# Kernel optimization log

Hardware: AMD Instinct MI355X
Metric: run time of the kernel (lower is better)

Reference implementation:

```python
import jax, jax.numpy as jnp
import numpy as np

A, B, O, C = 8, 32768, 256, 64   # num_agents, batch, obs_size, action_size
E, H = 128, 4                     # embedding_dim, attention_heads
Dh = E // H                       # attend_dim = 32
EPS = 1e-5                        # BatchNorm1d eps
SLOPE = 0.01                      # LeakyReLU default negative slope


def lrelu(x):
    return jnp.where(x >= 0, x, SLOPE * x)


def batchnorm(x, gamma, beta):
    # x: [A,B,F]; training-mode BatchNorm1d per agent (biased batch variance)
    mu = x.mean(axis=1, keepdims=True)
    var = x.var(axis=1, keepdims=True)
    return (x - mu) / jnp.sqrt(var + EPS) * gamma[:, None, :] + beta[:, None, :]


def setup_inputs() -> dict:
    key = jax.random.key(0)
    ks = jax.random.split(key, 13)
    s = lambda k, shape: jax.random.normal(k, shape, jnp.float32) * 0.05
    return {
        "observation_vector": jax.random.normal(ks[0], (A, B, O), jnp.float32),
        "action_vector": jax.random.normal(ks[1], (A, B, C), jnp.float32),
        "g_bn_gamma": jnp.ones((A, O + C), jnp.float32),
        "g_bn_beta": jnp.zeros((A, O + C), jnp.float32),
        "g_W": s(ks[2], (A, E, O + C)), "g_b": s(ks[3], (A, E)),
        "s_bn_gamma": jnp.ones((A, O), jnp.float32),
        "s_bn_beta": jnp.zeros((A, O), jnp.float32),
        "s_W": s(ks[4], (A, E, O)), "s_b": s(ks[5], (A, E)),
        "f_W1": s(ks[6], (A, E, 2 * E)), "f_b1": s(ks[7], (A, E)),
        "f_W2": s(ks[8], (A, C, E)), "f_b2": s(ks[9], (A, C)),
        "Wq": s(ks[10], (H, Dh, E)), "Wk": s(ks[11], (H, Dh, E)),
        "V": s(ks[12], (H, Dh, E)),
    }


def reference(observation_vector, action_vector, g_bn_gamma, g_bn_beta, g_W, g_b,
              s_bn_gamma, s_bn_beta, s_W, s_b, f_W1, f_b1, f_W2, f_b2, Wq, Wk, V):
    # per-agent embeddings of (obs, act) and obs-only
    combined = jnp.concatenate([observation_vector, action_vector], axis=2)      # [A,B,O+C]
    e = lrelu(jnp.einsum('abf,aef->abe', batchnorm(combined, g_bn_gamma, g_bn_beta), g_W)
              + g_b[:, None, :])                                                  # [A,B,E]
    si = lrelu(jnp.einsum('abf,aef->abe',
                          batchnorm(observation_vector, s_bn_gamma, s_bn_beta), s_W)
               + s_b[:, None, :])                                                 # [A,B,E]
    # NOTE: original applies F.softmax over a (batch,1) tensor -> every attention
    # weight is exactly 1.0, so x_i = sum_{j!=i} leaky_relu(V_l @ e_j). Wq/Wk only
    # feed the regularization logits (not returned when regularize=False).
    v = lrelu(jnp.einsum('abe,hde->abhd', e, V))                                  # [A,B,H,Dh]
    x = (v.sum(axis=0, keepdims=True) - v).reshape(A, B, E)                       # heads concatenated
    h = lrelu(jnp.einsum('abf,aef->abe', jnp.concatenate([x, si], axis=2), f_W1)
              + f_b1[:, None, :])                                                 # [A,B,E]
    q_all = jnp.einsum('abe,ace->abc', h, f_W2) + f_b2[:, None, :]                # [A,B,C]
    ids = jnp.argmax(action_vector, axis=2)[..., None]                            # [A,B,1]
    return jnp.take_along_axis(q_all, ids, axis=2)                                # [A,B,1]
```

## Files before the change

### kernel.cpp

```cpp
#include <hip/hip_runtime.h>
#include <hip/hip_bf16.h>
#include <stdint.h>

constexpr int A_ = 8, B_ = 32768, O_ = 256, C_ = 64, F_ = 320, E_ = 128;
constexpr int NCH = 128, CHROWS = B_ / NCH;
constexpr int NBT = B_ / 16;

typedef __attribute__((ext_vector_type(8))) __bf16 bf16x8;
typedef __attribute__((ext_vector_type(4))) float f32x4;
union U4 { uint4 u; bf16x8 v; __bf16 b[8]; };

__device__ __forceinline__ float lrelu(float x){ return x >= 0.f ? x : 0.01f*x; }
__device__ __forceinline__ f32x4 mfma16(bf16x8 a, bf16x8 b, f32x4 c){
  return __builtin_amdgcn_mfma_f32_16x16x32_bf16(a, b, c, 0, 0, 0);
}
__device__ __forceinline__ bf16x8 pk8(f32x4 lo, f32x4 hi){
  U4 r;
  r.b[0]=(__bf16)lo[0]; r.b[1]=(__bf16)lo[1]; r.b[2]=(__bf16)lo[2]; r.b[3]=(__bf16)lo[3];
  r.b[4]=(__bf16)hi[0]; r.b[5]=(__bf16)hi[1]; r.b[6]=(__bf16)hi[2]; r.b[7]=(__bf16)hi[3];
  return r.v;
}
__device__ __forceinline__ bf16x8 pk8f(float4 a, float4 b){
  U4 r;
  r.b[0]=(__bf16)a.x; r.b[1]=(__bf16)a.y; r.b[2]=(__bf16)a.z; r.b[3]=(__bf16)a.w;
  r.b[4]=(__bf16)b.x; r.b[5]=(__bf16)b.y; r.b[6]=(__bf16)b.z; r.b[7]=(__bf16)b.w;
  return r.v;
}
__device__ __forceinline__ void gl_lds16(const void* g, void* s){
  __builtin_amdgcn_global_load_lds(
      (const __attribute__((address_space(1))) unsigned int*)g,
      (__attribute__((address_space(3))) unsigned int*)s, 16, 0, 0);
}
template<int N> __device__ __forceinline__ void vmwait(){
  asm volatile("s_waitcnt vmcnt(%0)" :: "n"(N) : "memory");
}
__device__ __forceinline__ void lgkm0(){ asm volatile("s_waitcnt lgkmcnt(0)" ::: "memory"); }
__device__ __forceinline__ void sbar(){ __builtin_amdgcn_s_barrier(); }
__device__ __forceinline__ void schb(){ __builtin_amdgcn_sched_barrier(0); }

__global__ void k_stats_partial(const float* __restrict__ obs,
                                const float* __restrict__ act,
                                float* __restrict__ psum, float* __restrict__ psq,
                                int* __restrict__ ids){
  const int f = threadIdx.x, ch = blockIdx.x, a = blockIdx.y;
  const size_t b0 = (size_t)ch * CHROWS;
  float s = 0.f, q = 0.f;
  if (f < O_){
    const float* p = obs + ((size_t)a*B_ + b0)*O_ + f;
    for (int i = 0; i < CHROWS; ++i){ float x = p[(size_t)i*O_]; s += x; q += x*x; }
  } else {
    const float* p = act + ((size_t)a*B_ + b0)*C_ + (f - O_);
    for (int i = 0; i < CHROWS; ++i){ float x = p[(size_t)i*C_]; s += x; q += x*x; }
  }
  psum[((size_t)a*NCH + ch)*F_ + f] = s;
  psq [((size_t)a*NCH + ch)*F_ + f] = q;
  if (f < CHROWS){
    const float4* ar = (const float4*)(act + ((size_t)a*B_ + b0 + f)*C_);
    float best = -3.4e38f; int bi = 0;
    #pragma unroll 4
    for (int j = 0; j < 16; ++j){
      const float4 v = ar[j];
      const int c0 = j*4;
      if (v.x > best){ best = v.x; bi = c0;   }
      if (v.y > best){ best = v.y; bi = c0+1; }
      if (v.z > best){ best = v.z; bi = c0+2; }
      if (v.w > best){ best = v.w; bi = c0+3; }
    }
    ids[(size_t)a*B_ + b0 + f] = bi;
  }
}

__global__ void k_stats_final(const float* __restrict__ psum, const float* __restrict__ psq,
                              float* __restrict__ zscale, float* __restrict__ zshift){
  const int f = threadIdx.x, a = blockIdx.x;
  float s = 0.f, q = 0.f;
  for (int ch = 0; ch < NCH; ++ch){
    s += psum[((size_t)a*NCH + ch)*F_ + f];
    q += psq [((size_t)a*NCH + ch)*F_ + f];
  }
  const float mean = s * (1.0f / B_);
  float var = q * (1.0f / B_) - mean * mean;
  var = fmaxf(var, 0.0f);
  const float rs = rsqrtf(var + 1e-5f);
  zscale[a*F_ + f] = rs;
  zshift[a*F_ + f] = -mean * rs;
}

__global__ void k_prep_pack(const float* __restrict__ gW, const float* __restrict__ ggam,
                            const float* __restrict__ sW, const float* __restrict__ sgam,
                            const float* __restrict__ f1W, const float* __restrict__ f2W,
                            const float* __restrict__ Vm, const float* __restrict__ zscale,
                            __bf16* __restrict__ Ap, __bf16* __restrict__ Vp,
                            __bf16* __restrict__ B1p, __bf16* __restrict__ B2p){
  const int a = blockIdx.y;
  const int t0 = blockIdx.x*256 + threadIdx.x;
  constexpr int STR = 32*256;
  for (int i = t0; i < 10*16*64*8; i += STR){
    const int ks = i >> 13, mO = (i>>9)&15, l = (i>>3)&63, e = i&7;
    const int lg = l>>4, fo = mO*16 + (l&15), k = ks*32 + lg*8 + e;
    const float sc = zscale[a*F_ + k];
    float v;
    if (fo < 128) v = gW[(size_t)a*E_*F_ + (size_t)fo*F_ + k] * ggam[a*F_+k] * sc;
    else          v = (k < O_) ? sW[(size_t)a*E_*O_ + (size_t)(fo-128)*O_ + k] * sgam[a*O_+k] * sc : 0.f;
    Ap[(size_t)a*(10*16*64*8) + i] = (__bf16)v;
  }
  for (int i = t0; i < 8*8*64*8; i += STR){
    const int ks = i >> 12, mH = (i>>9)&7, l = (i>>3)&63, e = i&7;
    const int lg = l>>4, h = mH*16 + (l&15);
    const int f = 32*ks + 16*(e>>2) + 4*lg + (e&3);
    B1p[(size_t)a*(8*8*64*8) + i] = (__bf16)f1W[(size_t)a*E_*2*E_ + (size_t)h*2*E_ + f];
  }
  for (int i = t0; i < 4*4*64*8; i += STR){
    const int ks = i >> 11, mC = (i>>9)&3, l = (i>>3)&63, e = i&7;
    const int lg = l>>4, c = mC*16 + (l&15);
    const int f = 32*ks + 16*(e>>2) + 4*lg + (e&3);
    B2p[(size_t)a*(4*4*64*8) + i] = (__bf16)f2W[(size_t)a*C_*E_ + (size_t)c*E_ + f];
  }
  if (a == 0){
    for (int i = t0; i < 4*8*64*8; i += STR){
      const int ks = i >> 12, mV = (i>>9)&7, l = (i>>3)&63, e = i&7;
      const int lg = l>>4, vo = mV*16 + (l&15);
      const int f = 32*ks + 16*(e>>2) + 4*lg + (e&3);
      Vp[i] = (__bf16)Vm[(size_t)vo*E_ + f];
    }
  }
}

__global__ void k_prep_bias(const float* __restrict__ gW, const float* __restrict__ gb,
                            const float* __restrict__ ggam, const float* __restrict__ gbet,
                            const float* __restrict__ sW, const float* __restrict__ sb,
                            const float* __restrict__ sgam, const float* __restrict__ sbet,
                            const float* __restrict__ zshift, float* __restrict__ gsb){
  __shared__ float ww[F_];
  __shared__ float part[2][128];
  const int a = blockIdx.y, t = threadIdx.x;
  const int o = t & 127, h = t >> 7;
  if (blockIdx.x == 0){
    for (int f = t; f < F_; f += 256)
      ww[f] = gbet[a*F_+f] + ggam[a*F_+f]*zshift[a*F_+f];
    __syncthreads();
    float s = 0.f;
    #pragma unroll 4
    for (int f = h*160; f < h*160 + 160; f += 4){
      const float4 wv = *(const float4*)&gW[(size_t)a*E_*F_ + (size_t)o*F_ + f];
      s += wv.x*ww[f] + wv.y*ww[f+1] + wv.z*ww[f+2] + wv.w*ww[f+3];
    }
    part[h][o] = s;
    __syncthreads();
    if (t < 128) gsb[a*256 + t] = gb[a*E_+t] + part[0][t] + part[1][t];
  } else {
    for (int f = t; f < O_; f += 256)
      ww[f] = sbet[a*O_+f] + sgam[a*O_+f]*zshift[a*F_+f];
    __syncthreads();
    float s = 0.f;
    #pragma unroll 4
    for (int f = h*128; f < h*128 + 128; f += 4){
      const float4 wv = *(const float4*)&sW[(size_t)a*E_*O_ + (size_t)o*O_ + f];
      s += wv.x*ww[f] + wv.y*ww[f+1] + wv.z*ww[f+2] + wv.w*ww[f+3];
    }
    part[h][o] = s;
    __syncthreads();
    if (t < 128) gsb[a*256 + 128 + t] = sb[a*E_+t] + part[0][t] + part[1][t];
  }
}

__global__ __launch_bounds__(256, 2) void k_stageA(
    const float* __restrict__ obs, const float* __restrict__ act,
    const __bf16* __restrict__ Ap, const __bf16* __restrict__ Vp,
    const float* __restrict__ gsb,
    uint4* __restrict__ si_q, uint4* __restrict__ v_q){
  constexpr int BUF = 26624;
  __shared__ __align__(16) char smem[2*BUF];
  const int a = (A_-1) - blockIdx.y;
  const int t = threadIdx.x;
  const int w = t>>6, l = t&63, l15 = l&15, lg = l>>4;
  const int bt0 = ((NBT/8 - 1) - blockIdx.x)*8;
  const size_t grow0 = (size_t)a*B_ + (size_t)bt0*16;
  const char* ApA = (const char*)Ap + (size_t)a*163840;
  const int xr = t>>1, kc0 = (t&1)*2;
  const float* obsrow = obs + (grow0 + xr)*O_;
  const float* actrow = act + (grow0 + xr)*C_;

  float4 xA[4], xB[4];

  auto wstage = [&](int ks, char* buf){
    const char* src = ApA + ks*16384;
    #pragma unroll
    for (int i = 0; i < 4; ++i)
      gl_lds16(src + (w*4+i)*1024 + l*16, buf + (w*4+i)*1024);
  };
  auto xload = [&](int ks, float4* d){
    const float* s = (ks < 8) ? (obsrow + ks*32 + kc0*8) : (actrow + (ks-8)*32 + kc0*8);
    d[0] = ((const float4*)s)[0]; d[1] = ((const float4*)s)[1];
    d[2] = ((const float4*)s)[2]; d[3] = ((const float4*)s)[3];
  };
  auto xwrite = [&](char* buf, const float4* d){
    *(bf16x8*)(buf + 16384 + xr*80 + kc0*16)     = pk8f(d[0], d[1]);
    *(bf16x8*)(buf + 16384 + xr*80 + (kc0+1)*16) = pk8f(d[2], d[3]);
  };

  f32x4 acc[4][8] = {};

  wstage(0, smem); schb();
  xload(0, xA);
  vmwait<0>();
  xwrite(smem, xA);
  xload(1, xB);
  lgkm0(); sbar(); schb();

  #pragma unroll
  for (int ks = 0; ks < 10; ++ks){
    char* cur = smem + (ks&1)*BUF;
    char* nxt = smem + ((ks+1)&1)*BUF;
    if (ks+1 < 10){ wstage(ks+1, nxt); schb(); }
    if (ks+2 < 10) xload(ks+2, (ks&1) ? xB : xA);
    {
      const bf16x8* wc = (const bf16x8*)cur;
      const char* xb = cur + 16384;
      bf16x8 bfr[8];
      #pragma unroll
      for (int nt = 0; nt < 8; ++nt)
        bfr[nt] = *(const bf16x8*)(xb + (nt*16 + l15)*80 + lg*16);
      #pragma unroll
      for (int m = 0; m < 4; ++m){
        const bf16x8 af = wc[(w*4+m)*64 + l];
        #pragma unroll
        for (int nt = 0; nt < 8; ++nt)
          acc[m][nt] = mfma16(af, bfr[nt], acc[m][nt]);
      }
    }
    schb();
    if (ks <= 7)      vmwait<4>();
    else if (ks == 8) vmwait<0>();
    if (ks+1 < 10) xwrite(nxt, (ks&1) ? xA : xB);
    if (ks < 9){ lgkm0(); sbar(); schb(); }
  }

  const float* bE = gsb + a*256 + w*64 + lg*4;
  #pragma unroll
  for (int m = 0; m < 4; ++m){
    const float4 b = *(const float4*)(bE + m*16);
    #pragma unroll
    for (int nt = 0; nt < 8; ++nt){
      acc[m][nt][0] = lrelu(acc[m][nt][0] + b.x);
      acc[m][nt][1] = lrelu(acc[m][nt][1] + b.y);
      acc[m][nt][2] = lrelu(acc[m][nt][2] + b.z);
      acc[m][nt][3] = lrelu(acc[m][nt][3] + b.w);
    }
  }
  sbar();

  if (w < 2){
    #pragma unroll
    for (int jp = 0; jp < 2; ++jp){
      const int kv = 2*w + jp;
      #pragma unroll
      for (int nt = 0; nt < 8; ++nt)
        *(bf16x8*)(smem + ((kv*8 + nt)*64 + l)*16) = pk8(acc[2*jp][nt], acc[2*jp+1][nt]);
    }
  } else {
    #pragma unroll
    for (int jp = 0; jp < 2; ++jp){
      const int j = 2*(w-2) + jp;
      #pragma unroll
      for (int nt = 0; nt < 8; ++nt){
        U4 u; u.v = pk8(acc[2*jp][nt], acc[2*jp+1][nt]);
        si_q[(((size_t)a*NBT + bt0 + nt)*4 + j)*64 + l] = u.u;
      }
    }
  }
  lgkm0(); sbar(); schb();

  const uint4* Vq = (const uint4*)Vp;
  f32x4 accv[2][8] = {};
  #pragma unroll
  for (int kv = 0; kv < 4; ++kv){
    U4 a0, a1;
    a0.u = Vq[(kv*8 + w*2 + 0)*64 + l];
    a1.u = Vq[(kv*8 + w*2 + 1)*64 + l];
    bf16x8 bv[8];
    #pragma unroll
    for (int nt = 0; nt < 8; ++nt)
      bv[nt] = *(const bf16x8*)(smem + ((kv*8 + nt)*64 + l)*16);
    #pragma unroll
    for (int nt = 0; nt < 8; ++nt){
      accv[0][nt] = mfma16(a0.v, bv[nt], accv[0][nt]);
      accv[1][nt] = mfma16(a1.v, bv[nt], accv[1][nt]);
    }
  }
  #pragma unroll
  for (int nt = 0; nt < 8; ++nt){
    f32x4 lo, hi;
    #pragma unroll
    for (int e = 0; e < 4; ++e){ lo[e] = lrelu(accv[0][nt][e]); hi[e] = lrelu(accv[1][nt][e]); }
    U4 u; u.v = pk8(lo, hi);
    v_q[(((size_t)a*NBT + bt0 + nt)*4 + w)*64 + l] = u.u;
  }
}

__global__ void k_vsum(const uint4* __restrict__ v_q, uint4* __restrict__ vsum_q){
  const size_t i = (size_t)blockIdx.x*256 + threadIdx.x;
  const size_t per_a = (size_t)NBT*4*64;
  float s[8] = {0,0,0,0,0,0,0,0};
  #pragma unroll
  for (int aa = 0; aa < 8; ++aa){
    U4 u; u.u = v_q[aa*per_a + i];
    #pragma unroll
    for (int e = 0; e < 8; ++e) s[e] += (float)u.b[e];
  }
  U4 o;
  #pragma unroll
  for (int e = 0; e < 8; ++e) o.b[e] = (__bf16)s[e];
  vsum_q[i] = o.u;
}

__global__ __launch_bounds__(256, 2) void k_stageC(
    const uint4* __restrict__ v_q, const uint4* __restrict__ si_q,
    const uint4* __restrict__ vsum_q,
    const __bf16* __restrict__ B1p, const __bf16* __restrict__ B2p,
    const float* __restrict__ f1b, const float* __restrict__ f2b,
    const int* __restrict__ ids, float* __restrict__ out){
  __shared__ __align__(16) char wsm[2*8192];
  __shared__ float qs[4][64][17];
  const int a = blockIdx.y, t = threadIdx.x;
  const int w = t>>6, l = t&63, l15 = l&15, lg = l>>4;
  const int btw = blockIdx.x*8 + w*2;
  const char* B1A = (const char*)B1p + (size_t)a*65536;
  const size_t vbase = (size_t)a*NBT*4*64;

  uint4 qA[2], qB[2], sA[2], sB[2];

  auto wstage = [&](int ks, char* dst){
    const char* src = B1A + ks*8192;
    #pragma unroll
    for (int i = 0; i < 2; ++i)
      gl_lds16(src + (w*2+i)*1024 + l*16, dst + (w*2+i)*1024);
  };
  auto bload = [&](int ks, uint4* qv, uint4* sv){
    if (ks < 4){
      #pragma unroll
      for (int nt = 0; nt < 2; ++nt){
        const size_t idx = ((size_t)(btw+nt)*4 + ks)*64 + l;
        qv[nt] = v_q[vbase + idx];
        sv[nt] = vsum_q[idx];
      }
    } else {
      #pragma unroll
      for (int nt = 0; nt < 2; ++nt)
        qv[nt] = si_q[vbase + ((size_t)(btw+nt)*4 + (ks-4))*64 + l];
    }
  };
  auto bmake = [&](int ks, const uint4* qv, const uint4* sv, bf16x8* bf){
    if (ks < 4){
      #pragma unroll
      for (int nt = 0; nt < 2; ++nt){
        U4 s, v; s.u = sv[nt]; v.u = qv[nt];
        f32x4 lo, hi;
        #pragma unroll
        for (int e = 0; e < 4; ++e){
          lo[e] = (float)s.b[e]   - (float)v.b[e];
          hi[e] = (float)s.b[e+4] - (float)v.b[e+4];
        }
        bf[nt] = pk8(lo, hi);
      }
    } else {
      #pragma unroll
      for (int nt = 0; nt < 2; ++nt){ U4 u; u.u = qv[nt]; bf[nt] = u.v; }
    }
  };

  f32x4 hacc[8][2] = {};
  wstage(0, wsm); schb();
  bload(0, qA, sA); schb();
  bload(1, qB, sB);
  vmwait<4>();
  sbar(); schb();

  #pragma unroll
  for (int ks = 0; ks < 8; ++ks){
    bf16x8 bf[2];
    bmake(ks, (ks&1) ? qB : qA, (ks&1) ? sB : sA, bf);
    if (ks+1 < 8){ wstage(ks+1, wsm + ((ks+1)&1)*8192); schb(); }
    if (ks+2 < 8) bload(ks+2, (ks&1) ? qB : qA, (ks&1) ? sB : sA);
    {
      const bf16x8* wc = (const bf16x8*)(wsm + (ks&1)*8192);
      #pragma unroll
      for (int m = 0; m < 8; ++m){
        const bf16x8 af = wc[m*64 + l];
        hacc[m][0] = mfma16(af, bf[0], hacc[m][0]);
        hacc[m][1] = mfma16(af, bf[1], hacc[m][1]);
      }
    }
    schb();
    if (ks <= 1)      vmwait<4>();
    else if (ks <= 5) vmwait<2>();
    else if (ks == 6) vmwait<0>();
    if (ks < 7){ sbar(); schb(); }
  }

  bf16x8 hb[4][2];
  const float* bH = f1b + a*E_ + lg*4;
  #pragma unroll
  for (int kq = 0; kq < 4; ++kq){
    const float4 b0v = *(const float4*)(bH + (2*kq)*16);
    const float4 b1v = *(const float4*)(bH + (2*kq+1)*16);
    #pragma unroll
    for (int nt = 0; nt < 2; ++nt){
      f32x4 lo, hi;
      lo[0]=lrelu(hacc[2*kq][nt][0]+b0v.x); lo[1]=lrelu(hacc[2*kq][nt][1]+b0v.y);
      lo[2]=lrelu(hacc[2*kq][nt][2]+b0v.z); lo[3]=lrelu(hacc[2*kq][nt][3]+b0v.w);
      hi[0]=lrelu(hacc[2*kq+1][nt][0]+b1v.x); hi[1]=lrelu(hacc[2*kq+1][nt][1]+b1v.y);
      hi[2]=lrelu(hacc[2*kq+1][nt][2]+b1v.z); hi[3]=lrelu(hacc[2*kq+1][nt][3]+b1v.w);
      hb[kq][nt] = pk8(lo, hi);
    }
  }
  const uint4* A2q = (const uint4*)(B2p + (size_t)a*(4*4*64*8));
  f32x4 accq[4][2] = {};
  #pragma unroll
  for (int kq = 0; kq < 4; ++kq){
    #pragma unroll
    for (int mC = 0; mC < 4; ++mC){
      U4 af; af.u = A2q[(kq*4 + mC)*64 + l];
      accq[mC][0] = mfma16(af.v, hb[kq][0], accq[mC][0]);
      accq[mC][1] = mfma16(af.v, hb[kq][1], accq[mC][1]);
    }
  }
  const float* bQ = f2b + a*C_ + lg*4;
  float4 qb[4];
  #pragma unroll
  for (int mC = 0; mC < 4; ++mC) qb[mC] = *(const float4*)(bQ + mC*16);
  #pragma unroll
  for (int nt = 0; nt < 2; ++nt){
    #pragma unroll
    for (int mC = 0; mC < 4; ++mC){
      qs[w][mC*16 + lg*4 + 0][l15] = accq[mC][nt][0] + qb[mC].x;
      qs[w][mC*16 + lg*4 + 1][l15] = accq[mC][nt][1] + qb[mC].y;
      qs[w][mC*16 + lg*4 + 2][l15] = accq[mC][nt][2] + qb[mC].z;
      qs[w][mC*16 + lg*4 + 3][l15] = accq[mC][nt][3] + qb[mC].w;
    }
    lgkm0();
    if (l < 16){
      const size_t row = (size_t)(btw + nt)*16 + l;
      const int id = ids[(size_t)a*B_ + row];
      out[(size_t)a*B_ + row] = qs[w][id][l];
    }
    lgkm0();
  }
}

extern "C" void kernel_launch(void* const* d_in, const int* in_sizes, int n_in,
                              void* d_out, int out_size, void* d_ws, size_t ws_size,
                              hipStream_t stream) {
  const float* obs  = (const float*)d_in[0];
  const float* act  = (const float*)d_in[1];
  const float* ggam = (const float*)d_in[2];
  const float* gbet = (const float*)d_in[3];
  const float* gW   = (const float*)d_in[4];
  const float* gb   = (const float*)d_in[5];
  const float* sgam = (const float*)d_in[6];
  const float* sbet = (const float*)d_in[7];
  const float* sW   = (const float*)d_in[8];
  const float* sb   = (const float*)d_in[9];
  const float* f1W  = (const float*)d_in[10];
  const float* f1b  = (const float*)d_in[11];
  const float* f2W  = (const float*)d_in[12];
  const float* f2b  = (const float*)d_in[13];
  const float* Vm   = (const float*)d_in[16];
  float* out = (float*)d_out;

  char* base = (char*)d_ws; size_t off = 0;
  auto alloc = [&](size_t bytes) -> void* {
    off = (off + 255) & ~(size_t)255; void* p = base + off; off += bytes; return p;
  };
  float* psum    = (float*)alloc((size_t)A_*NCH*F_*4);
  float* psq     = (float*)alloc((size_t)A_*NCH*F_*4);
  float* zscale  = (float*)alloc((size_t)A_*F_*4);
  float* zshift  = (float*)alloc((size_t)A_*F_*4);
  float* gsb     = (float*)alloc((size_t)A_*256*4);
  __bf16* Ap     = (__bf16*)alloc((size_t)A_*10*16*64*8*2);
  __bf16* Vp     = (__bf16*)alloc((size_t)4*8*64*8*2);
  __bf16* B1p    = (__bf16*)alloc((size_t)A_*8*8*64*8*2);
  __bf16* B2p    = (__bf16*)alloc((size_t)A_*4*4*64*8*2);
  uint4* si_q    = (uint4*)alloc((size_t)A_*NBT*4*64*16);
  uint4* v_q     = (uint4*)alloc((size_t)A_*NBT*4*64*16);
  uint4* vsum_q  = (uint4*)alloc((size_t)NBT*4*64*16);
  int*   ids     = (int*)alloc((size_t)A_*B_*4);
  (void)ws_size; (void)in_sizes; (void)n_in; (void)out_size;

  k_stats_partial<<<dim3(NCH, A_), 320, 0, stream>>>(obs, act, psum, psq, ids);
  k_stats_final<<<A_, F_, 0, stream>>>(psum, psq, zscale, zshift);
  k_prep_pack<<<dim3(32, A_), 256, 0, stream>>>(gW, ggam, sW, sgam, f1W, f2W, Vm,
                                                zscale, Ap, Vp, B1p, B2p);
  k_prep_bias<<<dim3(2, A_), 256, 0, stream>>>(gW, gb, ggam, gbet, sW, sb, sgam, sbet,
                                               zshift, gsb);
  k_stageA<<<dim3(NBT/8, A_), 256, 0, stream>>>(obs, act, Ap, Vp, gsb, si_q, v_q);
  k_vsum<<<(NBT*4*64)/256, 256, 0, stream>>>(v_q, vsum_q);
  k_stageC<<<dim3(NBT/8, A_), 256, 0, stream>>>(v_q, si_q, vsum_q, B1p, B2p,
                                                f1b, f2b, ids, out);
}
```

Before: 257.1 us.

## Replace hand-tuned software pipelining with simple syncthreads-based loops

Stage A drops the two-deep register prefetch of activations, the explicit vmcnt waits and the sched barriers, and uses one register buffer plus __syncthreads each step. Stage C drops LDS staging of the f_W1 weights and the register double buffering, and reads weights and activations straight from global memory inside the k loop. This makes the code simpler and lowers LDS use, but it gives up explicit overlap of memory latency with MFMA work. It also adds full block barriers in the output gather.

```diff
diff --git a/kernel.cpp b/kernel.cpp
--- a/kernel.cpp
+++ b/kernel.cpp
@@ -31,12 +31,6 @@
       (const __attribute__((address_space(1))) unsigned int*)g,
       (__attribute__((address_space(3))) unsigned int*)s, 16, 0, 0);
 }
-template<int N> __device__ __forceinline__ void vmwait(){
-  asm volatile("s_waitcnt vmcnt(%0)" :: "n"(N) : "memory");
-}
-__device__ __forceinline__ void lgkm0(){ asm volatile("s_waitcnt lgkmcnt(0)" ::: "memory"); }
-__device__ __forceinline__ void sbar(){ __builtin_amdgcn_s_barrier(); }
-__device__ __forceinline__ void schb(){ __builtin_amdgcn_sched_barrier(0); }
 
 __global__ void k_stats_partial(const float* __restrict__ obs,
                                 const float* __restrict__ act,
@@ -181,7 +175,7 @@
   const float* obsrow = obs + (grow0 + xr)*O_;
   const float* actrow = act + (grow0 + xr)*C_;
 
-  float4 xA[4], xB[4];
+  float4 xr4[4];
 
   auto wstage = [&](int ks, char* buf){
     const char* src = ApA + ks*16384;
@@ -201,19 +195,19 @@
 
   f32x4 acc[4][8] = {};
 
-  wstage(0, smem); schb();
-  xload(0, xA);
-  vmwait<0>();
-  xwrite(smem, xA);
-  xload(1, xB);
-  lgkm0(); sbar(); schb();
+  wstage(0, smem);
+  xload(0, xr4);
+  xwrite(smem, xr4);
+  __syncthreads();
 
   #pragma unroll
   for (int ks = 0; ks < 10; ++ks){
     char* cur = smem + (ks&1)*BUF;
     char* nxt = smem + ((ks+1)&1)*BUF;
-    if (ks+1 < 10){ wstage(ks+1, nxt); schb(); }
-    if (ks+2 < 10) xload(ks+2, (ks&1) ? xB : xA);
+    if (ks+1 < 10){
+      wstage(ks+1, nxt);
+      xload(ks+1, xr4);
+    }
     {
       const bf16x8* wc = (const bf16x8*)cur;
       const char* xb = cur + 16384;
@@ -229,11 +223,8 @@
           acc[m][nt] = mfma16(af, bfr[nt], acc[m][nt]);
       }
     }
-    schb();
-    if (ks <= 7)      vmwait<4>();
-    else if (ks == 8) vmwait<0>();
-    if (ks+1 < 10) xwrite(nxt, (ks&1) ? xA : xB);
-    if (ks < 9){ lgkm0(); sbar(); schb(); }
+    if (ks+1 < 10) xwrite(nxt, xr4);
+    __syncthreads();
   }
 
   const float* bE = gsb + a*256 + w*64 + lg*4;
@@ -248,8 +239,6 @@
       acc[m][nt][3] = lrelu(acc[m][nt][3] + b.w);
     }
   }
-  sbar();
-
   if (w < 2){
     #pragma unroll
     for (int jp = 0; jp < 2; ++jp){
@@ -269,7 +258,7 @@
       }
     }
   }
-  lgkm0(); sbar(); schb();
+  __syncthreads();
 
   const uint4* Vq = (const uint4*)Vp;
   f32x4 accv[2][8] = {};
@@ -320,41 +309,22 @@
     const __bf16* __restrict__ B1p, const __bf16* __restrict__ B2p,
     const float* __restrict__ f1b, const float* __restrict__ f2b,
     const int* __restrict__ ids, float* __restrict__ out){
-  __shared__ __align__(16) char wsm[2*8192];
   __shared__ float qs[4][64][17];
   const int a = blockIdx.y, t = threadIdx.x;
   const int w = t>>6, l = t&63, l15 = l&15, lg = l>>4;
   const int btw = blockIdx.x*8 + w*2;
-  const char* B1A = (const char*)B1p + (size_t)a*65536;
+  const uint4* B1q = (const uint4*)(B1p + (size_t)a*(8*8*64*8));
   const size_t vbase = (size_t)a*NBT*4*64;
 
-  uint4 qA[2], qB[2], sA[2], sB[2];
-
-  auto wstage = [&](int ks, char* dst){
-    const char* src = B1A + ks*8192;
-    #pragma unroll
-    for (int i = 0; i < 2; ++i)
-      gl_lds16(src + (w*2+i)*1024 + l*16, dst + (w*2+i)*1024);
-  };
-  auto bload = [&](int ks, uint4* qv, uint4* sv){
+  f32x4 hacc[8][2] = {};
+  #pragma unroll
+  for (int ks = 0; ks < 8; ++ks){
+    bf16x8 bf[2];
     if (ks < 4){
       #pragma unroll
       for (int nt = 0; nt < 2; ++nt){
         const size_t idx = ((size_t)(btw+nt)*4 + ks)*64 + l;
-        qv[nt] = v_q[vbase + idx];
-        sv[nt] = vsum_q[idx];
-      }
-    } else {
-      #pragma unroll
-      for (int nt = 0; nt < 2; ++nt)
-        qv[nt] = si_q[vbase + ((size_t)(btw+nt)*4 + (ks-4))*64 + l];
-    }
-  };
-  auto bmake = [&](int ks, const uint4* qv, const uint4* sv, bf16x8* bf){
-    if (ks < 4){
-      #pragma unroll
-      for (int nt = 0; nt < 2; ++nt){
-        U4 s, v; s.u = sv[nt]; v.u = qv[nt];
+        U4 s, v; v.u = v_q[vbase + idx]; s.u = vsum_q[idx];
         f32x4 lo, hi;
         #pragma unroll
         for (int e = 0; e < 4; ++e){
@@ -365,37 +335,17 @@
       }
     } else {
       #pragma unroll
-      for (int nt = 0; nt < 2; ++nt){ U4 u; u.u = qv[nt]; bf[nt] = u.v; }
-    }
-  };
-
-  f32x4 hacc[8][2] = {};
-  wstage(0, wsm); schb();
-  bload(0, qA, sA); schb();
-  bload(1, qB, sB);
-  vmwait<4>();
-  sbar(); schb();
-
-  #pragma unroll
-  for (int ks = 0; ks < 8; ++ks){
-    bf16x8 bf[2];
-    bmake(ks, (ks&1) ? qB : qA, (ks&1) ? sB : sA, bf);
-    if (ks+1 < 8){ wstage(ks+1, wsm + ((ks+1)&1)*8192); schb(); }
-    if (ks+2 < 8) bload(ks+2, (ks&1) ? qB : qA, (ks&1) ? sB : sA);
-    {
-      const bf16x8* wc = (const bf16x8*)(wsm + (ks&1)*8192);
-      #pragma unroll
-      for (int m = 0; m < 8; ++m){
-        const bf16x8 af = wc[m*64 + l];
-        hacc[m][0] = mfma16(af, bf[0], hacc[m][0]);
-        hacc[m][1] = mfma16(af, bf[1], hacc[m][1]);
+      for (int nt = 0; nt < 2; ++nt){
+        U4 u; u.u = si_q[vbase + ((size_t)(btw+nt)*4 + (ks-4))*64 + l];
+        bf[nt] = u.v;
       }
     }
-    schb();
-    if (ks <= 1)      vmwait<4>();
-    else if (ks <= 5) vmwait<2>();
-    else if (ks == 6) vmwait<0>();
-    if (ks < 7){ sbar(); schb(); }
+    #pragma unroll
+    for (int m = 0; m < 8; ++m){
+      U4 af; af.u = B1q[(ks*8 + m)*64 + l];
+      hacc[m][0] = mfma16(af.v, bf[0], hacc[m][0]);
+      hacc[m][1] = mfma16(af.v, bf[1], hacc[m][1]);
+    }
   }
 
   bf16x8 hb[4][2];
@@ -438,13 +388,13 @@
       qs[w][mC*16 + lg*4 + 2][l15] = accq[mC][nt][2] + qb[mC].z;
       qs[w][mC*16 + lg*4 + 3][l15] = accq[mC][nt][3] + qb[mC].w;
     }
-    lgkm0();
+    __syncthreads();
     if (l < 16){
       const size_t row = (size_t)(btw + nt)*16 + l;
       const int id = ids[(size_t)a*B_ + row];
       out[(size_t)a*B_ + row] = qs[w][id][l];
     }
-    lgkm0();
+    __syncthreads();
   }
 }
 
```

Result: slower. 318.8 us (+24.0%).
